# Kernel tuning notes

Hardware: AMD Instinct MI355X
Metric: run time of the kernel (lower is better)

The kernel has to match this reference:

```python
import jax, jax.numpy as jnp
import numpy as np

B, C, H, W = 4, 96, 64, 64
D_STATE, D_CONV, EXPAND = 16, 4, 2
D_INNER = EXPAND * C          # 192
DT_RANK = (C + 15) // 16      # 6
BN_EPS = 1e-5


def setup_inputs() -> dict:
    key = jax.random.key(0)
    ks = jax.random.split(key, 10)
    s = 0.02
    return {
        "x": jax.random.normal(ks[0], (B, C, H, W), jnp.float32),
        # Mamba block params (mamba_ssm layout, no bias on in/out proj)
        "in_proj_w": jax.random.normal(ks[1], (2 * D_INNER, C), jnp.float32) * s,
        "conv1d_w": jax.random.normal(ks[2], (D_INNER, 1, D_CONV), jnp.float32) * s,  # depthwise
        "conv1d_b": jnp.zeros((D_INNER,), jnp.float32),
        "x_proj_w": jax.random.normal(ks[3], (DT_RANK + 2 * D_STATE, D_INNER), jnp.float32) * s,
        "dt_proj_w": jax.random.normal(ks[4], (D_INNER, DT_RANK), jnp.float32) * s,
        "dt_proj_b": jax.random.normal(ks[5], (D_INNER,), jnp.float32) * s,
        "A_log": jnp.log(jnp.tile(jnp.arange(1, D_STATE + 1, dtype=jnp.float32), (D_INNER, 1))),
        "D": jnp.ones((D_INNER,), jnp.float32),
        "out_proj_w": jax.random.normal(ks[6], (C, D_INNER), jnp.float32) * s,
        # trailing ConvBNReLU6 params
        "conv2d_w": jax.random.normal(ks[7], (C, C, 3, 3), jnp.float32) * s,
        "bn_gamma": jnp.ones((C,), jnp.float32),
        "bn_beta": jnp.zeros((C,), jnp.float32),
        "bn_mean": jnp.zeros((C,), jnp.float32),
        "bn_var": jnp.ones((C,), jnp.float32),
    }


def _forward(x, in_proj_w, conv1d_w, conv1d_b, x_proj_w, dt_proj_w, dt_proj_b,
             A_log, D, out_proj_w, conv2d_w, bn_gamma, bn_beta, bn_mean, bn_var):
    b, c, h, w = x.shape
    L = h * w
    seq = x.reshape(b, c, L).transpose(0, 2, 1)              # [B, L, C] tokens
    xz = seq @ in_proj_w.T                                    # [B, L, 2*D_INNER]
    xi, z = jnp.split(xz, 2, axis=-1)

    # depthwise causal conv1d + SiLU
    xi_c = jax.lax.conv_general_dilated(
        xi.transpose(0, 2, 1), conv1d_w, (1,), [(D_CONV - 1, 0)],
        dimension_numbers=("NCH", "OIH", "NCH"), feature_group_count=D_INNER)
    xi = jax.nn.silu((xi_c + conv1d_b[None, :, None]).transpose(0, 2, 1))  # [B, L, D_INNER]

    # input-dependent dt, B, C
    x_dbl = xi @ x_proj_w.T                                   # [B, L, DT_RANK + 2*D_STATE]
    dt, Bm, Cm = jnp.split(x_dbl, [DT_RANK, DT_RANK + D_STATE], axis=-1)
    dt = jax.nn.softplus(dt @ dt_proj_w.T + dt_proj_b)        # [B, L, D_INNER]

    # discretize: dA = exp(dt*A), dBx = dt*B*x
    A = -jnp.exp(A_log)                                       # [D_INNER, D_STATE]
    dA = jnp.exp(dt[..., None] * A)                           # [B, L, D_INNER, D_STATE]
    dBx = dt[..., None] * Bm[:, :, None, :] * xi[..., None]   # [B, L, D_INNER, D_STATE]

    def step(hst, inputs):
        dA_t, dBx_t, C_t = inputs
        hst = dA_t * hst + dBx_t                              # [B, D_INNER, D_STATE]
        y_t = jnp.einsum("bds,bs->bd", hst, C_t)
        return hst, y_t

    h0 = jnp.zeros((b, D_INNER, D_STATE), xi.dtype)
    _, ys = jax.lax.scan(step, h0,
                         (dA.transpose(1, 0, 2, 3), dBx.transpose(1, 0, 2, 3), Cm.transpose(1, 0, 2)))
    y = ys.transpose(1, 0, 2)                                 # [B, L, D_INNER]
    y = (y + xi * D) * jax.nn.silu(z)                         # skip D + gate
    out = y @ out_proj_w.T                                    # [B, L, C]
    xm = out.transpose(0, 2, 1).reshape(b, c, h, w)

    # ConvBNReLU: 3x3 conv (pad 1, no bias) -> BN (inference) -> ReLU6
    xo = jax.lax.conv_general_dilated(xm, conv2d_w, (1, 1), [(1, 1), (1, 1)],
                                      dimension_numbers=("NCHW", "OIHW", "NCHW"))
    inv = bn_gamma / jnp.sqrt(bn_var + BN_EPS)
    xo = xo * inv[None, :, None, None] + (bn_beta - bn_mean * inv)[None, :, None, None]
    return jnp.clip(xo, 0.0, 6.0)


def reference(x, in_proj_w, conv1d_w, conv1d_b, x_proj_w, dt_proj_w, dt_proj_b,
              A_log, D, out_proj_w, conv2d_w, bn_gamma, bn_beta, bn_mean, bn_var):
    return _forward(x, in_proj_w, conv1d_w, conv1d_b, x_proj_w, dt_proj_w, dt_proj_b,
                    A_log, D, out_proj_w, conv2d_w, bn_gamma, bn_beta, bn_mean, bn_var)
```

## Files before the change

### kernel.cpp

```cpp
#include <hip/hip_runtime.h>
#include <math.h>

#define LQ 4096
#define DI 192
#define DS 16
#define NCHUNK 64

__device__ __forceinline__ float siluf_(float v) { return v / (1.f + __expf(-v)); }
__device__ __forceinline__ float softplusf_(float v) { return v > 20.f ? v : log1pf(__expf(v)); }

template <int CTRL>
__device__ __forceinline__ float dpp_add16_(float x) {
    int y = __builtin_amdgcn_update_dpp(0, __float_as_int(x), CTRL, 0xf, 0xf, true);
    return x + __int_as_float(y);
}
template <int CTRL>
__device__ __forceinline__ float dpp_shift_(float x) {
    int y = __builtin_amdgcn_update_dpp(0, __float_as_int(x), CTRL, 0xf, 0xf, true);
    return __int_as_float(y);
}
__device__ __forceinline__ void async_g2l16_(const float* g, float* l) {
    __builtin_amdgcn_global_load_lds(
        (const __attribute__((address_space(1))) void*)g,
        (__attribute__((address_space(3))) void*)l, 16, 0, 0);
}
__device__ __forceinline__ void async_g2l4_(const float* g, float* l) {
    __builtin_amdgcn_global_load_lds(
        (const __attribute__((address_space(1))) void*)g,
        (__attribute__((address_space(3))) void*)l, 4, 0, 0);
}

__global__ __launch_bounds__(256) void k1_inproj(const float* __restrict__ x,
    const float* __restrict__ w, const float* __restrict__ cw,
    const float* __restrict__ cb, float* __restrict__ xi, float* __restrict__ z)
{
    const int l0 = blockIdx.x * 64;
    const int n0 = blockIdx.y * 64;
    const int b  = blockIdx.z;
    __shared__ float xs[96 * 64];
    __shared__ float wsT[96 * 68];
    const int tid = threadIdx.x;
    for (int i = tid; i < 96 * 16; i += 256) {
        int c = i >> 4, lq = i & 15;
        *(float4*)&xs[c * 64 + lq * 4] =
            *(const float4*)&x[(b * 96 + c) * LQ + l0 + lq * 4];
    }
    for (int i = tid; i < 64 * 24; i += 256) {
        int n = i / 24, cq = i - n * 24;
        float4 v = *(const float4*)&w[(n0 + n) * 96 + cq * 4];
        wsT[(cq * 4 + 0) * 68 + n] = v.x;
        wsT[(cq * 4 + 1) * 68 + n] = v.y;
        wsT[(cq * 4 + 2) * 68 + n] = v.z;
        wsT[(cq * 4 + 3) * 68 + n] = v.w;
    }
    __syncthreads();
    const int tx = tid & 15;
    const int ty = tid >> 4;
    float acc[4][4];
#pragma unroll
    for (int i = 0; i < 4; ++i)
#pragma unroll
        for (int j = 0; j < 4; ++j) acc[i][j] = 0.f;
    for (int k = 0; k < 96; ++k) {
        float4 a  = *(const float4*)&xs[k * 64 + ty * 4];
        float4 bb = *(const float4*)&wsT[k * 68 + tx * 4];
        float av[4] = {a.x, a.y, a.z, a.w};
        float bv[4] = {bb.x, bb.y, bb.z, bb.w};
#pragma unroll
        for (int i = 0; i < 4; ++i)
#pragma unroll
            for (int j = 0; j < 4; ++j) acc[i][j] += av[i] * bv[j];
    }
    if (n0 >= DI) {
#pragma unroll
        for (int i = 0; i < 4; ++i) {
            int l = l0 + ty * 4 + i;
            float4 v = make_float4(acc[i][0], acc[i][1], acc[i][2], acc[i][3]);
            *(float4*)&z[(b * LQ + l) * DI + (n0 - DI) + tx * 4] = v;
        }
        return;
    }
    __syncthreads();
    float* sxz = xs;
#pragma unroll
    for (int i = 0; i < 4; ++i) {
        int r = 3 + ty * 4 + i;
        *(float4*)&sxz[r * 64 + tx * 4] =
            make_float4(acc[i][0], acc[i][1], acc[i][2], acc[i][3]);
    }
    if (tid < 192) {
        int lh = tid >> 6;
        int nn = tid & 63;
        float a = 0.f;
        if (l0 > 0) {
            const float* xc = x + (size_t)b * 96 * LQ + (l0 - 3 + lh);
            for (int c = 0; c < 96; ++c)
                a += xc[c * LQ] * wsT[c * 68 + nn];
        }
        sxz[lh * 64 + nn] = a;
    }
    __syncthreads();
    {
        const int nn = tid & 63;
        const int lg = tid >> 6;
        const int d  = n0 + nn;
        float4 wv = *(const float4*)&cw[d * 4];
        float bias = cb[d];
#pragma unroll 4
        for (int p = 0; p < 16; ++p) {
            int l = lg + p * 4;
            float a = bias;
            a += wv.x * sxz[(l + 0) * 64 + nn];
            a += wv.y * sxz[(l + 1) * 64 + nn];
            a += wv.z * sxz[(l + 2) * 64 + nn];
            a += wv.w * sxz[(l + 3) * 64 + nn];
            xi[(b * LQ + l0 + l) * DI + d] = siluf_(a);
        }
    }
}

__global__ __launch_bounds__(256) void k3_xdbl(const float* __restrict__ xi,
    const float* __restrict__ xw, float* __restrict__ xdbl)
{
    const int l0 = blockIdx.x * 64;
    const int b  = blockIdx.y;
    __shared__ float sxiT[96 * 68];
    __shared__ float swx[38 * 196];
    const int tid = threadIdx.x;
    for (int i = tid; i < 38 * 48; i += 256) {
        int n = i / 48, kq = i - n * 48;
        *(float4*)&swx[n * 196 + kq * 4] = *(const float4*)&xw[n * 192 + kq * 4];
    }
    const int lq = tid & 15, ng = tid >> 4;
    float acc[3][4];
#pragma unroll
    for (int p = 0; p < 3; ++p)
#pragma unroll
        for (int i = 0; i < 4; ++i) acc[p][i] = 0.f;
    for (int half = 0; half < 2; ++half) {
        __syncthreads();
        for (int i = tid; i < 64 * 24; i += 256) {
            int l = i / 24, kq = i - l * 24;
            float4 v = *(const float4*)&xi[(b * LQ + l0 + l) * DI + half * 96 + kq * 4];
            sxiT[(kq * 4 + 0) * 68 + l] = v.x;
            sxiT[(kq * 4 + 1) * 68 + l] = v.y;
            sxiT[(kq * 4 + 2) * 68 + l] = v.z;
            sxiT[(kq * 4 + 3) * 68 + l] = v.w;
        }
        __syncthreads();
#pragma unroll
        for (int pass = 0; pass < 3; ++pass) {
            int n = pass * 16 + ng;
            if (n >= 38) continue;
            for (int k = 0; k < 96; ++k) {
                float4 a = *(const float4*)&sxiT[k * 68 + lq * 4];
                float bv = swx[n * 196 + half * 96 + k];
                acc[pass][0] += a.x * bv;
                acc[pass][1] += a.y * bv;
                acc[pass][2] += a.z * bv;
                acc[pass][3] += a.w * bv;
            }
        }
    }
#pragma unroll
    for (int pass = 0; pass < 3; ++pass) {
        int n = pass * 16 + ng;
        if (n >= 38) continue;
#pragma unroll
        for (int i = 0; i < 4; ++i)
            xdbl[(b * LQ + l0 + lq * 4 + i) * 38 + n] = acc[pass][i];
    }
}

__global__ __launch_bounds__(256) void k4_scanA(
    const float* __restrict__ xdbl, const float* __restrict__ xi,
    const float* __restrict__ dtw, const float* __restrict__ dtb,
    const float* __restrict__ alog,
    float* __restrict__ cA, float* __restrict__ cB)
{
    const int ch = blockIdx.x, g = blockIdx.y, b = blockIdx.z;
    const int t0 = ch * 64, d0 = g * 16;
    __shared__ float sxd[64 * 40];
    __shared__ float sdt[1024], sxi[1024];
    __shared__ float sdtw[96], sdtb[16];
    const int tid = threadIdx.x;
    for (int i = tid; i < 64 * 38; i += 256) {
        int t = i / 38, cc = i - t * 38;
        sxd[t * 40 + cc] = xdbl[(b * LQ + t0 + t) * 38 + cc];
    }
    for (int i = tid; i < 1024; i += 256) {
        int t = i >> 4, j = i & 15;
        sxi[i] = xi[(b * LQ + t0 + t) * DI + d0 + j];
    }
    if (tid < 96) sdtw[tid] = dtw[d0 * 6 + tid];
    if (tid < 16) sdtb[tid] = dtb[d0 + tid];
    __syncthreads();
    for (int i = tid; i < 1024; i += 256) {
        int t = i >> 4, dl = i & 15;
        float acc = sdtb[dl];
#pragma unroll
        for (int r = 0; r < 6; ++r) acc += sxd[t * 40 + r] * sdtw[dl * 6 + r];
        sdt[i] = softplusf_(acc);
    }
    __syncthreads();
    const int s = tid & 15, dl = tid >> 4;
    const float Ads = -__expf(alog[(d0 + dl) * DS + s]);
    float a = 1.f, hb = 0.f;
#pragma unroll 4
    for (int t = 0; t < 64; ++t) {
        float dtv = sdt[t * 16 + dl];
        float dA = __expf(dtv * Ads);
        float dbx = dtv * sxd[t * 40 + 6 + s] * sxi[t * 16 + dl];
        a *= dA;
        hb = dA * hb + dbx;
    }
    int o = ((b * NCHUNK + ch) * DI + d0 + dl) * DS + s;
    cA[o] = a;
    cB[o] = hb;
}

__global__ __launch_bounds__(256) void k5_combine(const float* __restrict__ cA,
    const float* __restrict__ cB, float* __restrict__ hinit)
{
    int gid = blockIdx.x * 256 + threadIdx.x;
    int b = gid / 3072;
    int rem = gid - b * 3072;
    int base = b * (NCHUNK * 3072) + rem;
    float h = 0.f;
#pragma unroll 8
    for (int c = 0; c < NCHUNK; ++c) {
        int o = base + c * 3072;
        hinit[o] = h;
        h = cA[o] * h + cB[o];
    }
}

__global__ __launch_bounds__(256) void k6_scanC(
    const float* __restrict__ xdbl, const float* __restrict__ xi,
    const float* __restrict__ z, const float* __restrict__ dtw,
    const float* __restrict__ dtb, const float* __restrict__ alog,
    const float* __restrict__ Dp, const float* __restrict__ hinit,
    float* __restrict__ yg)
{
    const int ch = blockIdx.x, g = blockIdx.y, b = blockIdx.z;
    const int t0 = ch * 64, d0 = g * 16;
    __shared__ float sxd[64 * 40];
    __shared__ float sdt[1024], sxi[1024], szs[1024], sy[1024];
    __shared__ float sdtw[96], sdtb[16];
    const int tid = threadIdx.x;
    for (int i = tid; i < 64 * 38; i += 256) {
        int t = i / 38, cc = i - t * 38;
        sxd[t * 40 + cc] = xdbl[(b * LQ + t0 + t) * 38 + cc];
    }
    for (int i = tid; i < 1024; i += 256) {
        int t = i >> 4, j = i & 15;
        int row = b * LQ + t0 + t;
        sxi[i] = xi[row * DI + d0 + j];
        szs[i] = z[row * DI + d0 + j];
    }
    if (tid < 96) sdtw[tid] = dtw[d0 * 6 + tid];
    if (tid < 16) sdtb[tid] = dtb[d0 + tid];
    __syncthreads();
    for (int i = tid; i < 1024; i += 256) {
        int t = i >> 4, dl = i & 15;
        float acc = sdtb[dl];
#pragma unroll
        for (int r = 0; r < 6; ++r) acc += sxd[t * 40 + r] * sdtw[dl * 6 + r];
        sdt[i] = softplusf_(acc);
    }
    __syncthreads();
    const int s = tid & 15, dl = tid >> 4;
    const float Ads = -__expf(alog[(d0 + dl) * DS + s]);
    float h = hinit[((b * NCHUNK + ch) * DI + d0 + dl) * DS + s];
    for (int t = 0; t < 64; ++t) {
        float dtv = sdt[t * 16 + dl];
        float dA = __expf(dtv * Ads);
        h = dA * h + dtv * sxd[t * 40 + 6 + s] * sxi[t * 16 + dl];
        float p = h * sxd[t * 40 + 22 + s];
        p = dpp_add16_<0x128>(p);
        p = dpp_add16_<0x124>(p);
        p = dpp_add16_<0x122>(p);
        p = dpp_add16_<0x121>(p);
        if (s == 0) sy[t * 16 + dl] = p;
    }
    __syncthreads();
    for (int i = tid; i < 1024; i += 256) {
        int t = i >> 4, j = i & 15;
        float gate = siluf_(szs[i]);
        yg[(b * LQ + t0 + t) * DI + d0 + j] = (sy[i] + sxi[i] * Dp[d0 + j]) * gate;
    }
}

__global__ __launch_bounds__(256) void k7_outproj(const float* __restrict__ yg,
    const float* __restrict__ wo, float* __restrict__ xm)
{
    const int l0 = blockIdx.x * 64;
    const int n0 = blockIdx.y * 32;
    const int b  = blockIdx.z;
    __shared__ float syT[96 * 68];
    __shared__ float wtT[192 * 36];
    const int tid = threadIdx.x;
    for (int i = tid; i < 32 * 48; i += 256) {
        int n = i / 48, kq = i - n * 48;
        float4 v = *(const float4*)&wo[(n0 + n) * DI + kq * 4];
        wtT[(kq * 4 + 0) * 36 + n] = v.x;
        wtT[(kq * 4 + 1) * 36 + n] = v.y;
        wtT[(kq * 4 + 2) * 36 + n] = v.z;
        wtT[(kq * 4 + 3) * 36 + n] = v.w;
    }
    const int tx = tid & 15;
    const int ty = tid >> 4;
    float acc[2][4];
#pragma unroll
    for (int j = 0; j < 2; ++j)
#pragma unroll
        for (int i = 0; i < 4; ++i) acc[j][i] = 0.f;
    for (int half = 0; half < 2; ++half) {
        __syncthreads();
        for (int i = tid; i < 64 * 24; i += 256) {
            int l = i / 24, kq = i - l * 24;
            float4 v = *(const float4*)&yg[(b * LQ + l0 + l) * DI + half * 96 + kq * 4];
            syT[(kq * 4 + 0) * 68 + l] = v.x;
            syT[(kq * 4 + 1) * 68 + l] = v.y;
            syT[(kq * 4 + 2) * 68 + l] = v.z;
            syT[(kq * 4 + 3) * 68 + l] = v.w;
        }
        __syncthreads();
        for (int k = 0; k < 96; ++k) {
            float4 a = *(const float4*)&syT[k * 68 + tx * 4];
            int kk = half * 96 + k;
            float b0 = wtT[kk * 36 + ty * 2 + 0];
            float b1 = wtT[kk * 36 + ty * 2 + 1];
            acc[0][0] += a.x * b0; acc[0][1] += a.y * b0;
            acc[0][2] += a.z * b0; acc[0][3] += a.w * b0;
            acc[1][0] += a.x * b1; acc[1][1] += a.y * b1;
            acc[1][2] += a.z * b1; acc[1][3] += a.w * b1;
        }
    }
#pragma unroll
    for (int j = 0; j < 2; ++j) {
        float4 v = make_float4(acc[j][0], acc[j][1], acc[j][2], acc[j][3]);
        *(float4*)&xm[(b * 96 + n0 + ty * 2 + j) * LQ + l0 + tx * 4] = v;
    }
}

#define K8_INQ 384
#define K8_WNEL 288
__global__ __launch_bounds__(256) void k8_conv3(const float* __restrict__ xm,
    const float* __restrict__ w2, const float* __restrict__ bng,
    const float* __restrict__ bnb, const float* __restrict__ bnm,
    const float* __restrict__ bnv, float* __restrict__ out)
{
    const int flat = blockIdx.x;
    const int xcd  = flat & 7;
    const int k    = flat >> 3;
    const int cog  = k % 12;
    const int ybh  = k / 12;
    const int yb   = ybh * 8 + xcd;
    const int y0   = (yb >> 2) * 4;
    const int b    = yb & 3;
    const int co0  = cog * 8;

    __shared__ float sin2[2][1536];
    __shared__ float swt2[2][288];
    const int tid = threadIdx.x;
    const int sx = tid & 15;
    const int sy = (tid >> 4) & 3;
    const int cq = tid >> 6;

    int in_goff[2];
    bool in_ok[2];
#pragma unroll
    for (int j = 0; j < 2; ++j) {
        int i = tid + j * 256;
        int ci  = i / 96;
        int rem = i - ci * 96;
        int row = rem >> 4;
        int qx  = rem & 15;
        int gy  = y0 + row - 1;
        bool ok = (i < K8_INQ) && gy >= 0 && gy < 64;
        in_ok[j]  = ok;
        in_goff[j] = ok ? (ci * 4096 + gy * 64 + qx * 4) : 0;
    }
    int w_goff[2];
#pragma unroll
    for (int j = 0; j < 2; ++j) {
        int i = tid + j * 256;
        int ci  = i / 72;
        int rem = i - ci * 72;
        int kk  = rem >> 3;
        int cl  = rem & 7;
        w_goff[j] = (i < K8_WNEL) ? (cl * 864 + ci * 9 + kk) : 0;
    }

    const float* xb = xm + (size_t)b * 96 * 4096;
    const float* wb = w2 + (size_t)co0 * 864;
    const float4 zero4 = make_float4(0.f, 0.f, 0.f, 0.f);

#pragma unroll
    for (int bu = 0; bu < 2; ++bu) {
        if (!in_ok[0]) *(float4*)&sin2[bu][tid * 4] = zero4;
        if (tid < 128 && !in_ok[1]) *(float4*)&sin2[bu][(256 + tid) * 4] = zero4;
    }

    {
        if (in_ok[0]) async_g2l16_(xb + in_goff[0], &sin2[0][cq * 256]);
        if (tid < 128 && in_ok[1]) async_g2l16_(xb + in_goff[1], &sin2[0][1024 + cq * 256]);
        async_g2l4_(wb + w_goff[0], &swt2[0][cq * 64]);
        if (tid < 32) async_g2l4_(wb + w_goff[1], &swt2[0][256]);
    }
    __syncthreads();

    float acc[2][4];
#pragma unroll
    for (int c = 0; c < 2; ++c)
#pragma unroll
        for (int x = 0; x < 4; ++x) acc[c][x] = 0.f;

#pragma clang loop unroll(disable)
    for (int ch = 0; ch < 24; ++ch) {
        if (ch < 23) {
            const int nb = (ch + 1) & 1;
            const float* gx = xb + (ch + 1) * 16384;
            const float* gw = wb + (ch + 1) * 36;
            if (in_ok[0]) async_g2l16_(gx + in_goff[0], &sin2[nb][cq * 256]);
            if (tid < 128 && in_ok[1]) async_g2l16_(gx + in_goff[1], &sin2[nb][1024 + cq * 256]);
            async_g2l4_(gw + w_goff[0], &swt2[nb][cq * 64]);
            if (tid < 32) async_g2l4_(gw + w_goff[1], &swt2[nb][256]);
        }

        const float* sc = sin2[ch & 1];
        const float* wc = swt2[ch & 1];
#pragma unroll
        for (int cii = 0; cii < 4; ++cii) {
            float w6[3][6];
#pragma unroll
            for (int r = 0; r < 3; ++r) {
                float4 v = *(const float4*)&sc[(cii * 6 + sy + r) * 64 + sx * 4];
                w6[r][0] = dpp_shift_<0x111>(v.w);
                w6[r][1] = v.x; w6[r][2] = v.y; w6[r][3] = v.z; w6[r][4] = v.w;
                w6[r][5] = dpp_shift_<0x101>(v.x);
            }
#pragma unroll
            for (int ky = 0; ky < 3; ++ky) {
#pragma unroll
                for (int kx = 0; kx < 3; ++kx) {
                    float2 wv = *(const float2*)&wc[(cii * 9 + ky * 3 + kx) * 8 + cq * 2];
#pragma unroll
                    for (int x = 0; x < 4; ++x) {
                        float pv = w6[ky][x + kx];
                        acc[0][x] = fmaf(pv, wv.x, acc[0][x]);
                        acc[1][x] = fmaf(pv, wv.y, acc[1][x]);
                    }
                }
            }
        }

        __syncthreads();
    }

    const int yy = y0 + sy;
#pragma unroll
    for (int j = 0; j < 2; ++j) {
        const int cc = co0 + cq * 2 + j;
        float inv = bng[cc] / sqrtf(bnv[cc] + 1e-5f);
        float add = bnb[cc] - bnm[cc] * inv;
        float4 o;
        o.x = fminf(fmaxf(acc[j][0] * inv + add, 0.f), 6.f);
        o.y = fminf(fmaxf(acc[j][1] * inv + add, 0.f), 6.f);
        o.z = fminf(fmaxf(acc[j][2] * inv + add, 0.f), 6.f);
        o.w = fminf(fmaxf(acc[j][3] * inv + add, 0.f), 6.f);
        *(float4*)&out[((size_t)(b * 96 + cc) * 64 + yy) * 64 + sx * 4] = o;
    }
}

extern "C" void kernel_launch(void* const* d_in, const int* in_sizes, int n_in,
                              void* d_out, int out_size, void* d_ws, size_t ws_size,
                              hipStream_t stream) {
    (void)in_sizes; (void)n_in; (void)out_size; (void)ws_size;
    const float* x    = (const float*)d_in[0];
    const float* w_in = (const float*)d_in[1];
    const float* cw   = (const float*)d_in[2];
    const float* cb   = (const float*)d_in[3];
    const float* xw   = (const float*)d_in[4];
    const float* dtw  = (const float*)d_in[5];
    const float* dtb  = (const float*)d_in[6];
    const float* alog = (const float*)d_in[7];
    const float* Dp   = (const float*)d_in[8];
    const float* wo   = (const float*)d_in[9];
    const float* w2   = (const float*)d_in[10];
    const float* bng  = (const float*)d_in[11];
    const float* bnb  = (const float*)d_in[12];
    const float* bnm  = (const float*)d_in[13];
    const float* bnv  = (const float*)d_in[14];

    float* ws = (float*)d_ws;
    float* yg     = ws;
    float* z      = ws + 3145728;
    float* xi     = ws + 6291456;
    float* xdbl   = ws + 9437184;
    float* cA     = ws + 10059776;
    float* cB     = ws + 10846208;
    float* hinit  = ws + 11632640;
    float* xm     = ws + 12419072;

    dim3 blk(256);
    k1_inproj<<<dim3(64, 6, 4), blk, 0, stream>>>(x, w_in, cw, cb, xi, z);
    k3_xdbl<<<dim3(64, 4), blk, 0, stream>>>(xi, xw, xdbl);
    k4_scanA<<<dim3(NCHUNK, 12, 4), blk, 0, stream>>>(xdbl, xi, dtw, dtb, alog, cA, cB);
    k5_combine<<<dim3(48), blk, 0, stream>>>(cA, cB, hinit);
    k6_scanC<<<dim3(NCHUNK, 12, 4), blk, 0, stream>>>(xdbl, xi, z, dtw, dtb, alog, Dp, hinit, yg);
    k7_outproj<<<dim3(64, 3, 4), blk, 0, stream>>>(yg, wo, xm);
    k8_conv3<<<dim3(768), blk, 0, stream>>>(xm, w2, bng, bnb, bnm, bnv, (float*)d_out);
}
```

Baseline: 271.1 us.

## Load conv3 weights as wave-uniform scalars and widen xdbl blocks to 512 threads

In the 3x3 conv kernel, weights are no longer staged through LDS with async loads. Each wave now reads its two output channels' weights directly from global memory at a wave-uniform address (readfirstlane), so they can become scalar loads. This removes LDS traffic and the weight staging instructions, at the cost of per-iteration global/scalar loads. Separately, the x_proj kernel is launched with 512 threads so each thread computes two output groups instead of three, raising parallelism per block.

```diff
diff --git a/kernel.cpp b/kernel.cpp
--- a/kernel.cpp
+++ b/kernel.cpp
@@ -23,11 +23,6 @@
     __builtin_amdgcn_global_load_lds(
         (const __attribute__((address_space(1))) void*)g,
         (__attribute__((address_space(3))) void*)l, 16, 0, 0);
-}
-__device__ __forceinline__ void async_g2l4_(const float* g, float* l) {
-    __builtin_amdgcn_global_load_lds(
-        (const __attribute__((address_space(1))) void*)g,
-        (__attribute__((address_space(3))) void*)l, 4, 0, 0);
 }
 
 __global__ __launch_bounds__(256) void k1_inproj(const float* __restrict__ x,
@@ -119,7 +114,7 @@
     }
 }
 
-__global__ __launch_bounds__(256) void k3_xdbl(const float* __restrict__ xi,
+__global__ __launch_bounds__(512) void k3_xdbl(const float* __restrict__ xi,
     const float* __restrict__ xw, float* __restrict__ xdbl)
 {
     const int l0 = blockIdx.x * 64;
@@ -127,19 +122,19 @@
     __shared__ float sxiT[96 * 68];
     __shared__ float swx[38 * 196];
     const int tid = threadIdx.x;
-    for (int i = tid; i < 38 * 48; i += 256) {
+    for (int i = tid; i < 38 * 48; i += 512) {
         int n = i / 48, kq = i - n * 48;
         *(float4*)&swx[n * 196 + kq * 4] = *(const float4*)&xw[n * 192 + kq * 4];
     }
     const int lq = tid & 15, ng = tid >> 4;
-    float acc[3][4];
-#pragma unroll
-    for (int p = 0; p < 3; ++p)
+    float acc[2][4];
+#pragma unroll
+    for (int p = 0; p < 2; ++p)
 #pragma unroll
         for (int i = 0; i < 4; ++i) acc[p][i] = 0.f;
     for (int half = 0; half < 2; ++half) {
         __syncthreads();
-        for (int i = tid; i < 64 * 24; i += 256) {
+        for (int i = tid; i < 64 * 24; i += 512) {
             int l = i / 24, kq = i - l * 24;
             float4 v = *(const float4*)&xi[(b * LQ + l0 + l) * DI + half * 96 + kq * 4];
             sxiT[(kq * 4 + 0) * 68 + l] = v.x;
@@ -149,8 +144,8 @@
         }
         __syncthreads();
 #pragma unroll
-        for (int pass = 0; pass < 3; ++pass) {
-            int n = pass * 16 + ng;
+        for (int pass = 0; pass < 2; ++pass) {
+            int n = pass * 32 + ng;
             if (n >= 38) continue;
             for (int k = 0; k < 96; ++k) {
                 float4 a = *(const float4*)&sxiT[k * 68 + lq * 4];
@@ -163,8 +158,8 @@
         }
     }
 #pragma unroll
-    for (int pass = 0; pass < 3; ++pass) {
-        int n = pass * 16 + ng;
+    for (int pass = 0; pass < 2; ++pass) {
+        int n = pass * 32 + ng;
         if (n >= 38) continue;
 #pragma unroll
         for (int i = 0; i < 4; ++i)
@@ -345,7 +340,6 @@
 }
 
 #define K8_INQ 384
-#define K8_WNEL 288
 __global__ __launch_bounds__(256) void k8_conv3(const float* __restrict__ xm,
     const float* __restrict__ w2, const float* __restrict__ bng,
     const float* __restrict__ bnb, const float* __restrict__ bnm,
@@ -362,7 +356,6 @@
     const int co0  = cog * 8;
 
     __shared__ float sin2[2][1536];
-    __shared__ float swt2[2][288];
     const int tid = threadIdx.x;
     const int sx = tid & 15;
     const int sy = (tid >> 4) & 3;
@@ -382,19 +375,9 @@
         in_ok[j]  = ok;
         in_goff[j] = ok ? (ci * 4096 + gy * 64 + qx * 4) : 0;
     }
-    int w_goff[2];
-#pragma unroll
-    for (int j = 0; j < 2; ++j) {
-        int i = tid + j * 256;
-        int ci  = i / 72;
-        int rem = i - ci * 72;
-        int kk  = rem >> 3;
-        int cl  = rem & 7;
-        w_goff[j] = (i < K8_WNEL) ? (cl * 864 + ci * 9 + kk) : 0;
-    }
 
     const float* xb = xm + (size_t)b * 96 * 4096;
-    const float* wb = w2 + (size_t)co0 * 864;
+    const float* wbu = w2 + (size_t)__builtin_amdgcn_readfirstlane(co0 + cq * 2) * 864;
     const float4 zero4 = make_float4(0.f, 0.f, 0.f, 0.f);
 
 #pragma unroll
@@ -406,8 +389,6 @@
     {
         if (in_ok[0]) async_g2l16_(xb + in_goff[0], &sin2[0][cq * 256]);
         if (tid < 128 && in_ok[1]) async_g2l16_(xb + in_goff[1], &sin2[0][1024 + cq * 256]);
-        async_g2l4_(wb + w_goff[0], &swt2[0][cq * 64]);
-        if (tid < 32) async_g2l4_(wb + w_goff[1], &swt2[0][256]);
     }
     __syncthreads();
 
@@ -422,17 +403,19 @@
         if (ch < 23) {
             const int nb = (ch + 1) & 1;
             const float* gx = xb + (ch + 1) * 16384;
-            const float* gw = wb + (ch + 1) * 36;
             if (in_ok[0]) async_g2l16_(gx + in_goff[0], &sin2[nb][cq * 256]);
             if (tid < 128 && in_ok[1]) async_g2l16_(gx + in_goff[1], &sin2[nb][1024 + cq * 256]);
-            async_g2l4_(gw + w_goff[0], &swt2[nb][cq * 64]);
-            if (tid < 32) async_g2l4_(gw + w_goff[1], &swt2[nb][256]);
         }
 
         const float* sc = sin2[ch & 1];
-        const float* wc = swt2[ch & 1];
 #pragma unroll
         for (int cii = 0; cii < 4; ++cii) {
+            float wA[9], wB[9];
+#pragma unroll
+            for (int t = 0; t < 9; ++t) {
+                wA[t] = wbu[ch * 36 + cii * 9 + t];
+                wB[t] = wbu[864 + ch * 36 + cii * 9 + t];
+            }
             float w6[3][6];
 #pragma unroll
             for (int r = 0; r < 3; ++r) {
@@ -445,12 +428,13 @@
             for (int ky = 0; ky < 3; ++ky) {
 #pragma unroll
                 for (int kx = 0; kx < 3; ++kx) {
-                    float2 wv = *(const float2*)&wc[(cii * 9 + ky * 3 + kx) * 8 + cq * 2];
+                    float wa = wA[ky * 3 + kx];
+                    float wb = wB[ky * 3 + kx];
 #pragma unroll
                     for (int x = 0; x < 4; ++x) {
                         float pv = w6[ky][x + kx];
-                        acc[0][x] = fmaf(pv, wv.x, acc[0][x]);
-                        acc[1][x] = fmaf(pv, wv.y, acc[1][x]);
+                        acc[0][x] = fmaf(pv, wa, acc[0][x]);
+                        acc[1][x] = fmaf(pv, wb, acc[1][x]);
                     }
                 }
             }
@@ -506,7 +490,7 @@
 
     dim3 blk(256);
     k1_inproj<<<dim3(64, 6, 4), blk, 0, stream>>>(x, w_in, cw, cb, xi, z);
-    k3_xdbl<<<dim3(64, 4), blk, 0, stream>>>(xi, xw, xdbl);
+    k3_xdbl<<<dim3(64, 4), dim3(512), 0, stream>>>(xi, xw, xdbl);
     k4_scanA<<<dim3(NCHUNK, 12, 4), blk, 0, stream>>>(xdbl, xi, dtw, dtb, alog, cA, cB);
     k5_combine<<<dim3(48), blk, 0, stream>>>(cA, cB, hinit);
     k6_scanC<<<dim3(NCHUNK, 12, 4), blk, 0, stream>>>(xdbl, xi, z, dtw, dtb, alog, Dp, hinit, yg);
```

After: 267.9 us. Within noise of the previous version (-1.2%).
